# Kernel optimization log

Hardware: AMD Instinct MI355X
Metric: run time of the kernel (lower is better)

The kernel has to match this reference:

```python
import jax, jax.numpy as jnp
import numpy as np
from jax import lax

LAM = 0.1
NUM_ITERS = 20
SIGNAL_LENGTH = 4096


def _conv1d_same(x, k):
    # x: [B, L], k: [K]. TF tf.nn.conv1d is cross-correlation with SAME padding
    # (pad_total = K-1, lo = (K-1)//2), which matches lax 'SAME'.
    return lax.conv_general_dilated(x[:, None, :], k[None, None, :],
                                    window_strides=(1,), padding='SAME')[:, 0, :]


def setup_inputs() -> dict:
    key = jax.random.key(0)
    ks = jax.random.split(key, 4)
    B, L, K, H = 4096, SIGNAL_LENGTH, 64, 256
    y = jax.random.normal(ks[0], (B, L), jnp.float32)
    thz_pulse = jax.random.normal(ks[1], (K,), jnp.float32)
    W1 = jax.random.normal(ks[2], (L, H), jnp.float32) * 0.02
    b1 = jnp.zeros((H,), jnp.float32)
    W2 = jax.random.normal(ks[3], (H, 1), jnp.float32) * 0.02
    b2 = jnp.zeros((1,), jnp.float32)
    return {"y": y, "thz_pulse": thz_pulse, "W1": W1, "b1": b1, "W2": W2, "b2": b2}


def reference(y, thz_pulse, W1, b1, W2, b2):
    # tf.reverse of the pulse + TF cross-correlation == convolution with the pulse
    kernel = thz_pulse[::-1]
    # L (Lipschitz const) was a non-trainable Variable: no gradient through it
    L_const = lax.stop_gradient(jnp.sum(thz_pulse * thz_pulse))
    theta = LAM / L_const
    B_term = _conv1d_same(y, kernel) / L_const  # [B, L], constant across iterations

    def step(x, _):
        c = B_term + x - _conv1d_same(x, kernel) / L_const
        x_new = jnp.sign(c) * jnp.maximum(jnp.abs(c) - theta, 0.0)  # soft-threshold
        return x_new, None

    x, _ = lax.scan(step, jnp.zeros_like(y), None, length=NUM_ITERS)

    features = jax.nn.relu(x @ W1 + b1)          # [B, 256]
    peak_pred = (features @ W2 + b2)[:, 0] * SIGNAL_LENGTH  # [B]
    return x, peak_pred
```

## Files before the change

### kernel.cpp

```cpp
#include <hip/hip_runtime.h>

typedef __attribute__((ext_vector_type(4))) float f32x4;
typedef __attribute__((ext_vector_type(16))) float f32x16;
typedef __attribute__((ext_vector_type(8))) short short8;
typedef __attribute__((ext_vector_type(4))) short short4v;

#define PADW(I) ((I) + ((I) >> 4))
#define WOFF(z) ((z) + ((z) >> 4))

constexpr int LROW = 4096;
constexpr int KW   = 64;
constexpr int HALO = 32;
constexpr int NLOG = LROW + 2 * HALO;
constexpr int XS_SIZE = PADW(NLOG - 1) + 1;

constexpr int AS    = 10384;
constexpr int SLOT  = 3 * AS;
constexpr int POOLB = 2 * SLOT;
static_assert(XS_SIZE * 4 <= SLOT, "f32 y stage fits in buf1 region");
static_assert(POOLB + 2 * KW * 4 <= 65536, "static LDS limit");

__device__ __forceinline__ float bfh2f(unsigned short h) {
  return __uint_as_float(((unsigned)h) << 16);
}
__device__ __forceinline__ unsigned short btrunc(float x) {
  return (unsigned short)(__float_as_uint(x) >> 16);
}
__device__ __forceinline__ void split3s(float x, unsigned short& h,
                                        unsigned short& m, unsigned short& l) {
  h = btrunc(x);
  float r1 = (x - bfh2f(h)) * 256.0f;
  m = btrunc(r1);
  float r2 = (r1 - bfh2f(m)) * 256.0f;
  l = btrunc(r2);
}
__device__ __forceinline__ float shrinkf(float c, float theta) {
  float a = fabsf(c) - theta;
  return (a > 0.0f) ? copysignf(a, c) : 0.0f;
}

__device__ __forceinline__ void conv_row(const float* __restrict__ xw,
                                         const float* __restrict__ kn,
                                         float acc[16]) {
#pragma unroll
  for (int e = 0; e < 16; ++e) acc[e] = 0.0f;
#pragma unroll
  for (int m = 0; m < 79; ++m) {
    float wv = xw[WOFF(1 + m)];
    const int jlo = (m - 15 > 0) ? (m - 15) : 0;
    const int jhi = (m < 63) ? m : 63;
#pragma unroll
    for (int j = jlo; j <= jhi; ++j) acc[m - j] = fmaf(kn[j], wv, acc[m - j]);
  }
}

__global__ __launch_bounds__(256, 2) void ista_mfma(
    const float* __restrict__ y, const float* __restrict__ pulse,
    float* __restrict__ xout) {
  __shared__ __align__(16) char pool[POOLB];
  __shared__ float pl[KW];
  __shared__ float knl[KW];

  const int t = threadIdx.x, w = t >> 6, l = t & 63;
  const int lq = l & 31;
  const int hi = l >> 5;
  const int row = blockIdx.x;

  if (t < KW) pl[t] = pulse[t];

#pragma unroll
  for (int a = 0; a < 3; ++a) {
    char* ab = pool + a * AS;
    if (t < 16) *(unsigned*)(ab + 4 * t) = 0u;
    if (t < 16) *(unsigned*)(ab + 10320 + 4 * t) = 0u;
  }

  float* yw = (float*)(pool + SLOT);
  if (t < HALO) { yw[PADW(t)] = 0.0f; yw[PADW(NLOG - HALO + t)] = 0.0f; }
  const float* yrow = y + (size_t)row * LROW;
#pragma unroll
  for (int q = 0; q < 4; ++q) {
    int i4 = q * 256 + t; float4 v = ((const float4*)yrow)[i4];
    yw[PADW(HALO + 4 * i4 + 0)] = v.x; yw[PADW(HALO + 4 * i4 + 1)] = v.y;
    yw[PADW(HALO + 4 * i4 + 2)] = v.z; yw[PADW(HALO + 4 * i4 + 3)] = v.w;
  }
  __syncthreads();

  float Lc = 0.0f;
#pragma unroll
  for (int j = 0; j < KW; ++j) Lc += pl[j] * pl[j];
  const float theta = 0.1f / Lc, invL = 1.0f / Lc;
  if (t < KW) knl[t] = pl[KW - 1 - t] * invL;

  short8 Ah[6], Am[6], Al[6];
#pragma unroll
  for (int kf = 0; kf < 6; ++kf) {
#pragma unroll
    for (int j = 0; j < 8; ++j) {
      int q = 16 * kf + 8 * hi + j, d = q - lq - 1;
      float v = (d >= 0 && d < 64) ? pl[63 - d] * invL : 0.0f;
      float vc = ((q == lq + 32) ? 1.0f : 0.0f) - v;
      unsigned short h, m, lo; split3s(vc, h, m, lo);
      Ah[kf][j] = (short)h; Am[kf][j] = (short)m; Al[kf][j] = (short)lo;
    }
  }
  __syncthreads();

  float bts[16];
  conv_row(yw + 17 * t, knl, bts);
  __syncthreads();

#pragma unroll
  for (int e = 0; e < 16; ++e) (yw + 17 * t)[WOFF(32 + e)] = bts[e];
  __syncthreads();

  f32x16 bt;
#pragma unroll
  for (int r = 0; r < 16; ++r) {
    const int e = (r & 3) + 8 * (r >> 2) + 4 * hi;
    bt[r] = yw[PADW(32 + 1024 * w + 32 * lq + e)];
  }
  __syncthreads();

#pragma unroll
  for (int a = 0; a < 3; ++a) {
    char* ab = pool + SLOT + a * AS;
    if (t < 16) *(unsigned*)(ab + 4 * t) = 0u;
    if (t < 16) *(unsigned*)(ab + 10320 + 4 * t) = 0u;
  }

  const int rbL = 80 * (32 * w + lq) + 16 * hi;
  const int wbL = 80 * (32 * w + lq + 1) + 8 * hi;
  constexpr float S8 = 1.0f / 256.0f, S16 = 1.0f / 65536.0f;

  {
    unsigned short hh[16], mm[16], ll[16];
#pragma unroll
    for (int i = 0; i < 16; ++i) {
      float xn = shrinkf(bt[i], theta);
      split3s(xn, hh[i], mm[i], ll[i]);
    }
    char* wpb = pool + SLOT;
#pragma unroll
    for (int g = 0; g < 4; ++g) {
      short4v h4, m4, l4;
#pragma unroll
      for (int i = 0; i < 4; ++i) {
        h4[i] = (short)hh[4 * g + i]; m4[i] = (short)mm[4 * g + i];
        l4[i] = (short)ll[4 * g + i];
      }
      char* wp = wpb + wbL + 16 * g;
      *(short4v*)(wp)          = h4;
      *(short4v*)(wp + AS)     = m4;
      *(short4v*)(wp + 2 * AS) = l4;
    }
  }
  __syncthreads();

  for (int it = 0; it < 19; ++it) {
    const int rs = (it & 1) ? 0 : SLOT, ws = SLOT - rs;
    const char* rp = pool + rs + rbL;
    f32x16 ah = bt, am = (f32x16)0.0f, al = (f32x16)0.0f;
#pragma unroll
    for (int kf = 0; kf < 6; ++kf) {
      const char* p = rp + (32 * kf + 16 * (kf >> 1));
      short8 xh = *(const short8*)(p);
      short8 xm = *(const short8*)(p + AS);
      short8 xl = *(const short8*)(p + 2 * AS);
      ah = __builtin_amdgcn_mfma_f32_32x32x16_bf16(Ah[kf], xh, ah, 0, 0, 0);
      am = __builtin_amdgcn_mfma_f32_32x32x16_bf16(Ah[kf], xm, am, 0, 0, 0);
      am = __builtin_amdgcn_mfma_f32_32x32x16_bf16(Am[kf], xh, am, 0, 0, 0);
      al = __builtin_amdgcn_mfma_f32_32x32x16_bf16(Ah[kf], xl, al, 0, 0, 0);
      al = __builtin_amdgcn_mfma_f32_32x32x16_bf16(Am[kf], xm, al, 0, 0, 0);
      al = __builtin_amdgcn_mfma_f32_32x32x16_bf16(Al[kf], xh, al, 0, 0, 0);
    }
    unsigned short hh[16], mm[16], ll[16];
#pragma unroll
    for (int i = 0; i < 16; ++i) {
      float c  = fmaf(S16, al[i], fmaf(S8, am[i], ah[i]));
      float xn = shrinkf(c, theta);
      split3s(xn, hh[i], mm[i], ll[i]);
    }
    char* wpb = pool + ws;
#pragma unroll
    for (int g = 0; g < 4; ++g) {
      short4v h4, m4, l4;
#pragma unroll
      for (int i = 0; i < 4; ++i) {
        h4[i] = (short)hh[4 * g + i]; m4[i] = (short)mm[4 * g + i];
        l4[i] = (short)ll[4 * g + i];
      }
      char* wp = wpb + wbL + 16 * g;
      *(short4v*)(wp)          = h4;
      *(short4v*)(wp + AS)     = m4;
      *(short4v*)(wp + 2 * AS) = l4;
    }
    __syncthreads();
  }

  {
    const int base = 32 * t + 64 + 16 * ((t + 2) >> 1);
    float o[16];
#pragma unroll
    for (int s = 0; s < 2; ++s) {
      const char* hp = pool + base + 16 * s;
      short8 hv = *(const short8*)(hp);
      short8 mv = *(const short8*)(hp + AS);
      short8 lv = *(const short8*)(hp + 2 * AS);
#pragma unroll
      for (int c2 = 0; c2 < 8; ++c2) {
        float xv = fmaf(S8, bfh2f((unsigned short)mv[c2]),
                        bfh2f((unsigned short)hv[c2]));
        o[8 * s + c2] = fmaf(S16, bfh2f((unsigned short)lv[c2]), xv);
      }
    }
    float4* xr = (float4*)(xout + (size_t)row * LROW + 16 * t);
#pragma unroll
    for (int s = 0; s < 4; ++s)
      xr[s] = make_float4(o[4 * s], o[4 * s + 1], o[4 * s + 2], o[4 * s + 3]);
  }
}

__device__ __forceinline__ unsigned short f2bf(float f) {
  unsigned u = __float_as_uint(f);
  u += 0x7fffu + ((u >> 16) & 1u);
  return (unsigned short)(u >> 16);
}

__global__ __launch_bounds__(256) void cast_w1(const float* __restrict__ W1,
                                               unsigned short* __restrict__ W1p) {
  const int kq = blockIdx.x;
  const int c  = threadIdx.x;
  short8 v;
#pragma unroll
  for (int j = 0; j < 8; ++j)
    v[j] = (short)f2bf(W1[(size_t)(kq * 8 + j) * 256 + c]);
  *(short8*)(W1p + ((size_t)kq * 256 + c) * 8) = v;
}

__global__ __launch_bounds__(256) void mlp_mfma(
    const float* __restrict__ x, const unsigned short* __restrict__ W1p,
    const float* __restrict__ b1, const float* __restrict__ W2,
    const float* __restrict__ b2, float* __restrict__ out1) {
  __shared__ short Ap[16 * 8 * 8];
  __shared__ short Bp[8 * 256 * 8];
  __shared__ float pr[4][16];

  const int t = threadIdx.x;
  const int w = t >> 6;
  const int l = t & 63;
  const int lrow = l & 15;
  const int lk   = l >> 4;
  const int row0 = blockIdx.x * 16;

  f32x4 acc[4];
#pragma unroll
  for (int n = 0; n < 4; ++n) acc[n] = (f32x4)0.0f;

  for (int kt = 0; kt < 64; ++kt) {
    __syncthreads();
    {
      const int r  = t >> 4;
      const int k4 = t & 15;
      const float4 v = *(const float4*)(x + (size_t)(row0 + r) * LROW + kt * 64 + k4 * 4);
      short4v a;
      a.x = (short)f2bf(v.x); a.y = (short)f2bf(v.y);
      a.z = (short)f2bf(v.z); a.w = (short)f2bf(v.w);
      const int kq = k4 >> 1, h = k4 & 1;
      *(short4v*)((char*)Ap + ((r * 8 + (kq ^ (r & 7))) * 16 + h * 8)) = a;
    }
    {
      const short8* src = (const short8*)(W1p + (size_t)kt * (8 * 256 * 8));
      short8* dst = (short8*)Bp;
#pragma unroll
      for (int i = 0; i < 8; ++i) dst[t + 256 * i] = src[t + 256 * i];
    }
    __syncthreads();
#pragma unroll
    for (int kf = 0; kf < 2; ++kf) {
      const int kq = kf * 4 + lk;
      short8 af = *(short8*)((char*)Ap + (lrow * 8 + (kq ^ (lrow & 7))) * 16);
#pragma unroll
      for (int n = 0; n < 4; ++n) {
        short8 bf = *(short8*)((char*)Bp + (kq * 256 + w * 64 + n * 16 + lrow) * 16);
        acc[n] = __builtin_amdgcn_mfma_f32_16x16x32_bf16(af, bf, acc[n], 0, 0, 0);
      }
    }
  }

  float s[4] = {0.0f, 0.0f, 0.0f, 0.0f};
#pragma unroll
  for (int n = 0; n < 4; ++n) {
    const int c = w * 64 + n * 16 + lrow;
    const float b1v = b1[c];
    const float w2v = W2[c];
#pragma unroll
    for (int i = 0; i < 4; ++i) {
      float f = acc[n][i] + b1v;
      f = fmaxf(f, 0.0f);
      s[i] = fmaf(f, w2v, s[i]);
    }
  }
#pragma unroll
  for (int off = 1; off < 16; off <<= 1) {
#pragma unroll
    for (int i = 0; i < 4; ++i) s[i] += __shfl_xor(s[i], off, 64);
  }
  if (lrow == 0) {
#pragma unroll
    for (int i = 0; i < 4; ++i) pr[w][lk * 4 + i] = s[i];
  }
  __syncthreads();
  if (t < 16) {
    out1[row0 + t] =
        (pr[0][t] + pr[1][t] + pr[2][t] + pr[3][t] + b2[0]) * (float)LROW;
  }
}

extern "C" void kernel_launch(void* const* d_in, const int* in_sizes, int n_in,
                              void* d_out, int out_size, void* d_ws, size_t ws_size,
                              hipStream_t stream) {
  const float* y     = (const float*)d_in[0];
  const float* pulse = (const float*)d_in[1];
  const float* W1    = (const float*)d_in[2];
  const float* b1    = (const float*)d_in[3];
  const float* W2    = (const float*)d_in[4];
  const float* b2    = (const float*)d_in[5];

  float* xout = (float*)d_out;
  float* out1 = xout + (size_t)LROW * LROW;
  unsigned short* W1p = (unsigned short*)d_ws;

  cast_w1<<<512, 256, 0, stream>>>(W1, W1p);
  ista_mfma<<<LROW, 256, 0, stream>>>(y, pulse, xout);
  mlp_mfma<<<LROW / 16, 256, 0, stream>>>(xout, W1p, b1, W2, b2, out1);
}
```

Baseline: 420.5 us.

## Interleave hi/mid/lo bf16 planes per chunk and shrink LDS for three blocks per CU

Replaces the three separate hi/mid/lo bf16 LDS planes with an interleaved layout: each 32-element chunk keeps its h, m and l parts together with a 200-byte stride. This cuts the LDS pool from about 62 KB to 52 KB, and launch bounds are raised to allow three blocks per CU. The goal is higher occupancy, so more MFMA work can hide LDS latency and barrier stalls. In exchange, each operand fetch is split into two 8-byte reads, which adds LDS instructions and may introduce bank conflicts. It also tightens the register budget under the higher occupancy target.

```diff
diff --git a/kernel.cpp b/kernel.cpp
--- a/kernel.cpp
+++ b/kernel.cpp
@@ -14,11 +14,9 @@
 constexpr int NLOG = LROW + 2 * HALO;
 constexpr int XS_SIZE = PADW(NLOG - 1) + 1;
 
-constexpr int AS    = 10384;
-constexpr int SLOT  = 3 * AS;
-constexpr int POOLB = 2 * SLOT;
-static_assert(XS_SIZE * 4 <= SLOT, "f32 y stage fits in buf1 region");
-static_assert(POOLB + 2 * KW * 4 <= 65536, "static LDS limit");
+constexpr int SLOT2 = 26000;
+constexpr int POOL2 = 2 * SLOT2;
+static_assert(XS_SIZE * 4 <= SLOT2, "f32 y stage fits in buf1 region");
 
 __device__ __forceinline__ float bfh2f(unsigned short h) {
   return __uint_as_float(((unsigned)h) << 16);
@@ -54,10 +52,10 @@
   }
 }
 
-__global__ __launch_bounds__(256, 2) void ista_mfma(
+__global__ __launch_bounds__(256, 3) void ista_mfma(
     const float* __restrict__ y, const float* __restrict__ pulse,
     float* __restrict__ xout) {
-  __shared__ __align__(16) char pool[POOLB];
+  __shared__ __align__(16) char pool[POOL2];
   __shared__ float pl[KW];
   __shared__ float knl[KW];
 
@@ -68,14 +66,10 @@
 
   if (t < KW) pl[t] = pulse[t];
 
-#pragma unroll
-  for (int a = 0; a < 3; ++a) {
-    char* ab = pool + a * AS;
-    if (t < 16) *(unsigned*)(ab + 4 * t) = 0u;
-    if (t < 16) *(unsigned*)(ab + 10320 + 4 * t) = 0u;
-  }
-
-  float* yw = (float*)(pool + SLOT);
+  if (t < 48) *(unsigned*)(pool + 4 * t) = 0u;
+  if (t < 48) *(unsigned*)(pool + 25800 + 4 * t) = 0u;
+
+  float* yw = (float*)(pool + SLOT2);
   if (t < HALO) { yw[PADW(t)] = 0.0f; yw[PADW(NLOG - HALO + t)] = 0.0f; }
   const float* yrow = y + (size_t)row * LROW;
 #pragma unroll
@@ -122,15 +116,11 @@
   }
   __syncthreads();
 
-#pragma unroll
-  for (int a = 0; a < 3; ++a) {
-    char* ab = pool + SLOT + a * AS;
-    if (t < 16) *(unsigned*)(ab + 4 * t) = 0u;
-    if (t < 16) *(unsigned*)(ab + 10320 + 4 * t) = 0u;
-  }
-
-  const int rbL = 80 * (32 * w + lq) + 16 * hi;
-  const int wbL = 80 * (32 * w + lq + 1) + 8 * hi;
+  if (t < 48) *(unsigned*)(pool + SLOT2 + 4 * t) = 0u;
+  if (t < 48) *(unsigned*)(pool + SLOT2 + 25800 + 4 * t) = 0u;
+
+  const int rbase = 200 * (32 * w + lq) + 16 * hi;
+  const int wbase = 200 * (32 * w + lq + 1) + 8 * hi;
   constexpr float S8 = 1.0f / 256.0f, S16 = 1.0f / 65536.0f;
 
   {
@@ -140,7 +130,7 @@
       float xn = shrinkf(bt[i], theta);
       split3s(xn, hh[i], mm[i], ll[i]);
     }
-    char* wpb = pool + SLOT;
+    char* wpb = pool + SLOT2 + wbase;
 #pragma unroll
     for (int g = 0; g < 4; ++g) {
       short4v h4, m4, l4;
@@ -149,24 +139,30 @@
         h4[i] = (short)hh[4 * g + i]; m4[i] = (short)mm[4 * g + i];
         l4[i] = (short)ll[4 * g + i];
       }
-      char* wp = wpb + wbL + 16 * g;
-      *(short4v*)(wp)          = h4;
-      *(short4v*)(wp + AS)     = m4;
-      *(short4v*)(wp + 2 * AS) = l4;
+      char* wp = wpb + 16 * g;
+      *(short4v*)(wp)       = h4;
+      *(short4v*)(wp + 64)  = m4;
+      *(short4v*)(wp + 128) = l4;
     }
   }
   __syncthreads();
 
   for (int it = 0; it < 19; ++it) {
-    const int rs = (it & 1) ? 0 : SLOT, ws = SLOT - rs;
-    const char* rp = pool + rs + rbL;
+    const int rs = (it & 1) ? 0 : SLOT2, ws = SLOT2 - rs;
+    const char* rp = pool + rs + rbase;
     f32x16 ah = bt, am = (f32x16)0.0f, al = (f32x16)0.0f;
 #pragma unroll
     for (int kf = 0; kf < 6; ++kf) {
-      const char* p = rp + (32 * kf + 16 * (kf >> 1));
-      short8 xh = *(const short8*)(p);
-      short8 xm = *(const short8*)(p + AS);
-      short8 xl = *(const short8*)(p + 2 * AS);
+      const char* p = rp + 200 * (kf >> 1) + 32 * (kf & 1);
+      short4v h0 = *(const short4v*)(p);
+      short4v h1 = *(const short4v*)(p + 8);
+      short4v m0 = *(const short4v*)(p + 64);
+      short4v m1 = *(const short4v*)(p + 72);
+      short4v l0 = *(const short4v*)(p + 128);
+      short4v l1 = *(const short4v*)(p + 136);
+      short8 xh = __builtin_shufflevector(h0, h1, 0, 1, 2, 3, 4, 5, 6, 7);
+      short8 xm = __builtin_shufflevector(m0, m1, 0, 1, 2, 3, 4, 5, 6, 7);
+      short8 xl = __builtin_shufflevector(l0, l1, 0, 1, 2, 3, 4, 5, 6, 7);
       ah = __builtin_amdgcn_mfma_f32_32x32x16_bf16(Ah[kf], xh, ah, 0, 0, 0);
       am = __builtin_amdgcn_mfma_f32_32x32x16_bf16(Ah[kf], xm, am, 0, 0, 0);
       am = __builtin_amdgcn_mfma_f32_32x32x16_bf16(Am[kf], xh, am, 0, 0, 0);
@@ -181,7 +177,7 @@
       float xn = shrinkf(c, theta);
       split3s(xn, hh[i], mm[i], ll[i]);
     }
-    char* wpb = pool + ws;
+    char* wpb = pool + ws + wbase;
 #pragma unroll
     for (int g = 0; g < 4; ++g) {
       short4v h4, m4, l4;
@@ -190,28 +186,28 @@
         h4[i] = (short)hh[4 * g + i]; m4[i] = (short)mm[4 * g + i];
         l4[i] = (short)ll[4 * g + i];
       }
-      char* wp = wpb + wbL + 16 * g;
-      *(short4v*)(wp)          = h4;
-      *(short4v*)(wp + AS)     = m4;
-      *(short4v*)(wp + 2 * AS) = l4;
+      char* wp = wpb + 16 * g;
+      *(short4v*)(wp)       = h4;
+      *(short4v*)(wp + 64)  = m4;
+      *(short4v*)(wp + 128) = l4;
     }
     __syncthreads();
   }
 
   {
-    const int base = 32 * t + 64 + 16 * ((t + 2) >> 1);
+    const int base = 200 * ((t + 2) >> 1) + 32 * (t & 1);
     float o[16];
 #pragma unroll
-    for (int s = 0; s < 2; ++s) {
-      const char* hp = pool + base + 16 * s;
-      short8 hv = *(const short8*)(hp);
-      short8 mv = *(const short8*)(hp + AS);
-      short8 lv = *(const short8*)(hp + 2 * AS);
-#pragma unroll
-      for (int c2 = 0; c2 < 8; ++c2) {
+    for (int s = 0; s < 4; ++s) {
+      const char* hp = pool + base + 8 * s;
+      short4v hv = *(const short4v*)(hp);
+      short4v mv = *(const short4v*)(hp + 64);
+      short4v lv = *(const short4v*)(hp + 128);
+#pragma unroll
+      for (int c2 = 0; c2 < 4; ++c2) {
         float xv = fmaf(S8, bfh2f((unsigned short)mv[c2]),
                         bfh2f((unsigned short)hv[c2]));
-        o[8 * s + c2] = fmaf(S16, bfh2f((unsigned short)lv[c2]), xv);
+        o[4 * s + c2] = fmaf(S16, bfh2f((unsigned short)lv[c2]), xv);
       }
     }
     float4* xr = (float4*)(xout + (size_t)row * LROW + 16 * t);
```

Result: slower. 457.6 us (+8.8%).
